# Kernel tuning notes

Measured on AMD Instinct MI355X. Metric: run time of the kernel, lower is better.

## Reference

```python
import jax, jax.numpy as jnp
import numpy as np

NUM_MOVIES = 100000
MOVIE_FEAT = 128
USER_FEAT = 128
BATCH = 16384
N_NBRS = 50
D0, D1, D2 = 256, 256, 128  # layer_dims


def setup_inputs() -> dict:
    key = jax.random.key(0)
    ks = jax.random.split(key, 16)
    inp = {
        "users": jax.random.normal(ks[0], (BATCH, USER_FEAT), jnp.float32),
        "pos_movies": jax.random.normal(ks[1], (BATCH, MOVIE_FEAT), jnp.float32),
        "neg_movies": jax.random.normal(ks[2], (BATCH, MOVIE_FEAT), jnp.float32),
        "user_ids": jax.random.randint(ks[3], (BATCH,), 0, BATCH),
        "pos_movie_ids": jax.random.randint(ks[4], (BATCH,), 0, NUM_MOVIES),
        "neg_movie_ids": jax.random.randint(ks[5], (BATCH,), 0, NUM_MOVIES),
        "nbr_ids": jax.random.randint(ks[6], (BATCH, N_NBRS), 0, NUM_MOVIES),
        # learned params / buffers
        "movie_table": jax.random.normal(ks[7], (NUM_MOVIES, MOVIE_FEAT), jnp.float32),
        "Wu": jax.random.normal(ks[8], (USER_FEAT, D0), jnp.float32) * (1.0 / np.sqrt(USER_FEAT)),
        "bu": jnp.zeros((D0,), jnp.float32),
        "Wm": jax.random.normal(ks[9], (MOVIE_FEAT, D0), jnp.float32) * (1.0 / np.sqrt(MOVIE_FEAT)),
        "bm": jnp.zeros((D0,), jnp.float32),
        "W1": jax.random.normal(ks[10], (D0, D1), jnp.float32) * (1.0 / np.sqrt(D0)),
        "b1": jnp.zeros((D1,), jnp.float32),
        "W2": jax.random.normal(ks[11], (D1, D2), jnp.float32) * (1.0 / np.sqrt(D1)),
        "b2": jnp.zeros((D2,), jnp.float32),
    }
    return inp


def reference(users, pos_movies, neg_movies, user_ids, pos_movie_ids, neg_movie_ids,
              nbr_ids, movie_table, Wu, bu, Wm, bm, W1, b1, W2, b2):
    # user_projection / movie_projection
    user_emb = users @ Wu + bu                      # [B, D0]
    movie_emb = movie_table @ Wm + bm               # [N, D0]
    pos_emb = movie_emb[pos_movie_ids]              # [B, D0]
    neg_emb = movie_emb[neg_movie_ids]              # [B, D0]
    # vectorized replacement of the per-user neighbor gather + mean loop
    nbr_mean = jnp.mean(movie_emb[nbr_ids], axis=1)  # [B, N_NBRS, D0] -> [B, D0]
    user_emb = user_emb + nbr_mean
    x = jnp.stack([user_emb, pos_emb, neg_emb], axis=0)  # [3, B, D0]
    x = jax.nn.relu(x @ W1 + b1)
    x = jax.nn.relu(x @ W2 + b2)
    return (x[0], x[1], x[2])
```

## Files before the change

kernel.cpp:

```cpp
#include <hip/hip_runtime.h>
#include <hip/hip_bf16.h>
#include <type_traits>

#define BATCH_N   16384
#define FEAT      128
#define NNBR      50
#define NUM_MOVIES_N 100000

typedef short  short8  __attribute__((ext_vector_type(8)));
typedef float  floatx4 __attribute__((ext_vector_type(4)));

__device__ __forceinline__ __hip_bfloat16 f2bf(float x) { return __float2bfloat16(x); }

__global__ __launch_bounds__(256) void conv_table(
    const float* __restrict__ t, __hip_bfloat16* __restrict__ tb) {
  size_t i = ((size_t)blockIdx.x * 256 + threadIdx.x) * 8;
  float4 v0 = *(const float4*)(t + i);
  float4 v1 = *(const float4*)(t + i + 4);
  __hip_bfloat16 o[8];
  o[0] = f2bf(v0.x); o[1] = f2bf(v0.y); o[2] = f2bf(v0.z); o[3] = f2bf(v0.w);
  o[4] = f2bf(v1.x); o[5] = f2bf(v1.y); o[6] = f2bf(v1.z); o[7] = f2bf(v1.w);
  *(short8*)(tb + i) = *(short8*)o;
}

__global__ __launch_bounds__(256) void prep_kernel(
    const float* __restrict__ Wu, const float* __restrict__ Wm,
    const float* __restrict__ W1, const float* __restrict__ W2,
    const float* __restrict__ bu, const float* __restrict__ bm,
    __hip_bfloat16* __restrict__ WcatT, __hip_bfloat16* __restrict__ WmT,
    __hip_bfloat16* __restrict__ W1T,  __hip_bfloat16* __restrict__ W2T,
    float* __restrict__ bc) {
  int idx = blockIdx.x * 256 + threadIdx.x;
  int n = idx & 255, k = idx >> 8;
  float v = (k < 128) ? Wu[k * 256 + n] : Wm[(k - 128) * 256 + n];
  WcatT[n * 256 + k] = f2bf(v);
  W1T[n * 256 + k]   = f2bf(W1[k * 256 + n]);
  if (k < 128) WmT[n * 128 + k] = f2bf(Wm[k * 256 + n]);
  if (idx < 32768) {
    int k2 = idx >> 7, n2 = idx & 127;
    W2T[n2 * 256 + k2] = f2bf(W2[k2 * 128 + n2]);
  }
  if (idx < 256) bc[idx] = bu[idx] + bm[idx];
}

__global__ __launch_bounds__(256) void gather_user(
    const float* __restrict__ users, const int* __restrict__ nbr_ids,
    const __hip_bfloat16* __restrict__ tb, __hip_bfloat16* __restrict__ A_user) {
  int row  = (blockIdx.x << 2) + (threadIdx.x >> 6);
  int lane = threadIdx.x & 63;
  const int* nb = nbr_ids + row * NNBR;
  float ax = 0.f, ay = 0.f;
  #pragma unroll 5
  for (int j = 0; j < NNBR; ++j) {
    int id = nb[j];
    __hip_bfloat162 v = ((const __hip_bfloat162*)(tb + (size_t)id * FEAT))[lane];
    ax += __bfloat162float(v.x); ay += __bfloat162float(v.y);
  }
  ax *= (1.f / NNBR); ay *= (1.f / NNBR);
  float2 uv = ((const float2*)(users + (size_t)row * FEAT))[lane];
  __hip_bfloat162* dst = (__hip_bfloat162*)(A_user + (size_t)row * (2 * FEAT));
  __hip_bfloat162 t0; t0.x = f2bf(uv.x); t0.y = f2bf(uv.y);
  __hip_bfloat162 t1; t1.x = f2bf(ax);   t1.y = f2bf(ay);
  dst[lane]      = t0;
  dst[64 + lane] = t1;
}

__global__ __launch_bounds__(256) void gather_pn(
    const int* __restrict__ pos_ids, const int* __restrict__ neg_ids,
    const __hip_bfloat16* __restrict__ tb, __hip_bfloat16* __restrict__ A_pn) {
  int row  = (blockIdx.x << 2) + (threadIdx.x >> 6);
  int lane = threadIdx.x & 63;
  int id = (row < BATCH_N) ? pos_ids[row] : neg_ids[row - BATCH_N];
  __hip_bfloat162 v = ((const __hip_bfloat162*)(tb + (size_t)id * FEAT))[lane];
  ((__hip_bfloat162*)(A_pn + (size_t)row * FEAT))[lane] = v;
}

template <int KDIM, int NDIM, bool RELU, typename OutT>
__global__ __launch_bounds__(256) void gemm_bf16(
    const __hip_bfloat16* __restrict__ A, const __hip_bfloat16* __restrict__ Wt,
    const float* __restrict__ bias, OutT* __restrict__ C) {
  __shared__ __hip_bfloat16 Al[128][40];
  __shared__ __hip_bfloat16 Bl[128][40];

  const int t    = threadIdx.x;
  const int lane = t & 63;
  const int wid  = t >> 6;
  const int wm   = wid & 1, wn = wid >> 1;
  const int quad = lane >> 4, lrow = lane & 15;
  const long m0  = (long)blockIdx.x * 128;
  const int  n0  = blockIdx.y * 128;

  const int c0 = t, c1 = t + 256;
  const int r0 = c0 >> 2, kc0 = (c0 & 3) * 8;
  const int r1 = c1 >> 2, kc1 = (c1 & 3) * 8;

  floatx4 acc[4][4] = {};

  for (int k0 = 0; k0 < KDIM; k0 += 32) {
    short8 a0 = *(const short8*)(A  + (m0 + r0) * KDIM + k0 + kc0);
    short8 a1 = *(const short8*)(A  + (m0 + r1) * KDIM + k0 + kc1);
    short8 b0 = *(const short8*)(Wt + (long)(n0 + r0) * KDIM + k0 + kc0);
    short8 b1 = *(const short8*)(Wt + (long)(n0 + r1) * KDIM + k0 + kc1);
    __syncthreads();
    *(short8*)&Al[r0][kc0] = a0;
    *(short8*)&Al[r1][kc1] = a1;
    *(short8*)&Bl[r0][kc0] = b0;
    *(short8*)&Bl[r1][kc1] = b1;
    __syncthreads();

    short8 af[4], bfr[4];
    #pragma unroll
    for (int i = 0; i < 4; ++i)
      af[i] = *(const short8*)&Al[wm * 64 + i * 16 + lrow][quad * 8];
    #pragma unroll
    for (int i = 0; i < 4; ++i)
      bfr[i] = *(const short8*)&Bl[wn * 64 + i * 16 + lrow][quad * 8];

    #pragma unroll
    for (int i = 0; i < 4; ++i)
      #pragma unroll
      for (int j = 0; j < 4; ++j)
        acc[i][j] = __builtin_amdgcn_mfma_f32_16x16x32_bf16(
            af[i], bfr[j], acc[i][j], 0, 0, 0);
  }

  #pragma unroll
  for (int i = 0; i < 4; ++i) {
    #pragma unroll
    for (int j = 0; j < 4; ++j) {
      int gcol = n0 + wn * 64 + j * 16 + lrow;
      float bv = bias[gcol];
      #pragma unroll
      for (int r = 0; r < 4; ++r) {
        long grow = m0 + wm * 64 + i * 16 + quad * 4 + r;
        float v = acc[i][j][r] + bv;
        if (RELU) v = fmaxf(v, 0.f);
        if constexpr (std::is_same<OutT, float>::value)
          C[grow * NDIM + gcol] = v;
        else
          C[grow * NDIM + gcol] = f2bf(v);
      }
    }
  }
}

extern "C" void kernel_launch(void* const* d_in, const int* in_sizes, int n_in,
                              void* d_out, int out_size, void* d_ws, size_t ws_size,
                              hipStream_t stream) {
  const float* users   = (const float*)d_in[0];
  const int*   pos_ids = (const int*)d_in[4];
  const int*   neg_ids = (const int*)d_in[5];
  const int*   nbr_ids = (const int*)d_in[6];
  const float* table   = (const float*)d_in[7];
  const float* Wu = (const float*)d_in[8];
  const float* bu = (const float*)d_in[9];
  const float* Wm = (const float*)d_in[10];
  const float* bm = (const float*)d_in[11];
  const float* W1 = (const float*)d_in[12];
  const float* b1 = (const float*)d_in[13];
  const float* W2 = (const float*)d_in[14];
  const float* b2 = (const float*)d_in[15];
  float* out = (float*)d_out;

  char* p = (char*)d_ws;
  auto carve = [&](size_t bytes) { char* r = p; p += (bytes + 255) & ~(size_t)255; return r; };
  __hip_bfloat16* tb     = (__hip_bfloat16*)carve((size_t)NUM_MOVIES_N * FEAT * 2);
  __hip_bfloat16* WcatT  = (__hip_bfloat16*)carve(256 * 256 * 2);
  __hip_bfloat16* WmT    = (__hip_bfloat16*)carve(256 * 128 * 2);
  __hip_bfloat16* W1T    = (__hip_bfloat16*)carve(256 * 256 * 2);
  __hip_bfloat16* W2T    = (__hip_bfloat16*)carve(128 * 256 * 2);
  float*          bc     = (float*)carve(256 * 4);
  __hip_bfloat16* A_user = (__hip_bfloat16*)carve((size_t)BATCH_N * 256 * 2);
  __hip_bfloat16* A_pn   = (__hip_bfloat16*)carve((size_t)2 * BATCH_N * 128 * 2);
  __hip_bfloat16* E      = (__hip_bfloat16*)carve((size_t)3 * BATCH_N * 256 * 2);
  __hip_bfloat16* H      = (__hip_bfloat16*)carve((size_t)3 * BATCH_N * 256 * 2);

  conv_table<<<NUM_MOVIES_N * FEAT / (256 * 8), 256, 0, stream>>>(table, tb);
  prep_kernel<<<256, 256, 0, stream>>>(Wu, Wm, W1, W2, bu, bm,
                                       WcatT, WmT, W1T, W2T, bc);
  gather_user<<<BATCH_N / 4, 256, 0, stream>>>(users, nbr_ids, tb, A_user);
  gather_pn<<<2 * BATCH_N / 4, 256, 0, stream>>>(pos_ids, neg_ids, tb, A_pn);

  gemm_bf16<256, 256, false, __hip_bfloat16>
      <<<dim3(BATCH_N / 128, 2), 256, 0, stream>>>(A_user, WcatT, bc, E);
  gemm_bf16<128, 256, false, __hip_bfloat16>
      <<<dim3(2 * BATCH_N / 128, 2), 256, 0, stream>>>(A_pn, WmT, bm,
                                                       E + (size_t)BATCH_N * 256);
  gemm_bf16<256, 256, true, __hip_bfloat16>
      <<<dim3(3 * BATCH_N / 128, 2), 256, 0, stream>>>(E, W1T, b1, H);
  gemm_bf16<256, 128, true, float>
      <<<dim3(3 * BATCH_N / 128, 1), 256, 0, stream>>>(H, W2T, b2, out);
}
```

Measured before the change: 218.3 us.

## Fuse pos/neg gather and three GEMM layers into one LDS-resident MLP kernel

Replaces the pos/neg gather kernel and the four separate GEMM launches with a single fused kernel. Each block holds a 64-row tile in LDS across projection, layer 1 and layer 2, and gathers pos/neg rows from the bf16 table inside the kernel. Intermediate E and H activations therefore never go to global memory, and several launches are removed. Weights are now read directly from global/L2 per MFMA fragment instead of being staged in LDS. An XOR swizzle is used for LDS indexing to avoid bank conflicts. The trade-off is heavier weight traffic from cache and 64 KB of LDS per block, which limits occupancy.

```diff
diff --git a/kernel.cpp b/kernel.cpp
--- a/kernel.cpp
+++ b/kernel.cpp
@@ -1,6 +1,5 @@
 #include <hip/hip_runtime.h>
 #include <hip/hip_bf16.h>
-#include <type_traits>
 
 #define BATCH_N   16384
 #define FEAT      128
@@ -11,6 +10,10 @@
 typedef float  floatx4 __attribute__((ext_vector_type(4)));
 
 __device__ __forceinline__ __hip_bfloat16 f2bf(float x) { return __float2bfloat16(x); }
+
+__device__ __forceinline__ int sw_idx(int r, int c) {
+  return (r << 8) + ((((c >> 3) ^ (r & 7)) << 3) | (c & 7));
+}
 
 __global__ __launch_bounds__(256) void conv_table(
     const float* __restrict__ t, __hip_bfloat16* __restrict__ tb) {
@@ -65,81 +68,142 @@
   dst[64 + lane] = t1;
 }
 
-__global__ __launch_bounds__(256) void gather_pn(
+__global__ __launch_bounds__(256, 2) void fused_mlp(
+    const __hip_bfloat16* __restrict__ A_user,
+    const __hip_bfloat16* __restrict__ tb,
     const int* __restrict__ pos_ids, const int* __restrict__ neg_ids,
-    const __hip_bfloat16* __restrict__ tb, __hip_bfloat16* __restrict__ A_pn) {
-  int row  = (blockIdx.x << 2) + (threadIdx.x >> 6);
-  int lane = threadIdx.x & 63;
-  int id = (row < BATCH_N) ? pos_ids[row] : neg_ids[row - BATCH_N];
-  __hip_bfloat162 v = ((const __hip_bfloat162*)(tb + (size_t)id * FEAT))[lane];
-  ((__hip_bfloat162*)(A_pn + (size_t)row * FEAT))[lane] = v;
-}
-
-template <int KDIM, int NDIM, bool RELU, typename OutT>
-__global__ __launch_bounds__(256) void gemm_bf16(
-    const __hip_bfloat16* __restrict__ A, const __hip_bfloat16* __restrict__ Wt,
-    const float* __restrict__ bias, OutT* __restrict__ C) {
-  __shared__ __hip_bfloat16 Al[128][40];
-  __shared__ __hip_bfloat16 Bl[128][40];
+    const __hip_bfloat16* __restrict__ WcatT,
+    const __hip_bfloat16* __restrict__ WmT,
+    const __hip_bfloat16* __restrict__ W1T,
+    const __hip_bfloat16* __restrict__ W2T,
+    const float* __restrict__ bc, const float* __restrict__ bmv,
+    const float* __restrict__ b1, const float* __restrict__ b2,
+    float* __restrict__ out) {
+  __shared__ __hip_bfloat16 A_lds[64 * 256];
+  __shared__ __hip_bfloat16 E_lds[64 * 256];
 
   const int t    = threadIdx.x;
-  const int lane = t & 63;
-  const int wid  = t >> 6;
+  const int lane = t & 63, wid = t >> 6;
   const int wm   = wid & 1, wn = wid >> 1;
   const int quad = lane >> 4, lrow = lane & 15;
-  const long m0  = (long)blockIdx.x * 128;
-  const int  n0  = blockIdx.y * 128;
-
-  const int c0 = t, c1 = t + 256;
-  const int r0 = c0 >> 2, kc0 = (c0 & 3) * 8;
-  const int r1 = c1 >> 2, kc1 = (c1 & 3) * 8;
-
-  floatx4 acc[4][4] = {};
-
-  for (int k0 = 0; k0 < KDIM; k0 += 32) {
-    short8 a0 = *(const short8*)(A  + (m0 + r0) * KDIM + k0 + kc0);
-    short8 a1 = *(const short8*)(A  + (m0 + r1) * KDIM + k0 + kc1);
-    short8 b0 = *(const short8*)(Wt + (long)(n0 + r0) * KDIM + k0 + kc0);
-    short8 b1 = *(const short8*)(Wt + (long)(n0 + r1) * KDIM + k0 + kc1);
-    __syncthreads();
-    *(short8*)&Al[r0][kc0] = a0;
-    *(short8*)&Al[r1][kc1] = a1;
-    *(short8*)&Bl[r0][kc0] = b0;
-    *(short8*)&Bl[r1][kc1] = b1;
-    __syncthreads();
-
-    short8 af[4], bfr[4];
-    #pragma unroll
-    for (int i = 0; i < 4; ++i)
-      af[i] = *(const short8*)&Al[wm * 64 + i * 16 + lrow][quad * 8];
-    #pragma unroll
-    for (int i = 0; i < 4; ++i)
-      bfr[i] = *(const short8*)&Bl[wn * 64 + i * 16 + lrow][quad * 8];
-
-    #pragma unroll
-    for (int i = 0; i < 4; ++i)
-      #pragma unroll
-      for (int j = 0; j < 4; ++j)
-        acc[i][j] = __builtin_amdgcn_mfma_f32_16x16x32_bf16(
-            af[i], bfr[j], acc[i][j], 0, 0, 0);
-  }
-
-  #pragma unroll
-  for (int i = 0; i < 4; ++i) {
+  const int s    = blockIdx.y;
+  const int m0   = blockIdx.x * 64;
+
+  if (s == 0) {
+    #pragma unroll
+    for (int c = 0; c < 8; ++c) {
+      int ch = t + c * 256;
+      int r = ch >> 5, kc = (ch & 31) << 3;
+      *(short8*)&A_lds[sw_idx(r, kc)] =
+          *(const short8*)(A_user + ((size_t)(m0 + r) << 8) + kc);
+    }
+  } else {
+    const int* ids = (s == 1) ? pos_ids : neg_ids;
+    #pragma unroll
+    for (int c = 0; c < 4; ++c) {
+      int ch = t + c * 256;
+      int r = ch >> 4, kc = (ch & 15) << 3;
+      int id = ids[m0 + r];
+      *(short8*)&A_lds[sw_idx(r, kc)] =
+          *(const short8*)(tb + ((size_t)id << 7) + kc);
+    }
+  }
+  __syncthreads();
+
+  const __hip_bfloat16* W0 = (s == 0) ? WcatT : WmT;
+  const float* bias0 = (s == 0) ? bc : bmv;
+  const int K0 = (s == 0) ? 256 : 128;
+
+  {
+    floatx4 acc[2][8] = {};
+    for (int k0 = 0; k0 < K0; k0 += 32) {
+      short8 af[2];
+      #pragma unroll
+      for (int i = 0; i < 2; ++i)
+        af[i] = *(const short8*)&A_lds[sw_idx(wm * 32 + i * 16 + lrow, k0 + quad * 8)];
+      #pragma unroll
+      for (int j = 0; j < 8; ++j) {
+        int n = wn * 128 + j * 16 + lrow;
+        short8 bf = *(const short8*)(W0 + (size_t)n * K0 + k0 + quad * 8);
+        #pragma unroll
+        for (int i = 0; i < 2; ++i)
+          acc[i][j] = __builtin_amdgcn_mfma_f32_16x16x32_bf16(af[i], bf, acc[i][j], 0, 0, 0);
+      }
+    }
+    #pragma unroll
+    for (int j = 0; j < 8; ++j) {
+      int col = wn * 128 + j * 16 + lrow;
+      float bv = bias0[col];
+      #pragma unroll
+      for (int i = 0; i < 2; ++i)
+        #pragma unroll
+        for (int r = 0; r < 4; ++r) {
+          int row = wm * 32 + i * 16 + quad * 4 + r;
+          E_lds[sw_idx(row, col)] = f2bf(acc[i][j][r] + bv);
+        }
+    }
+  }
+  __syncthreads();
+
+  {
+    floatx4 acc[2][8] = {};
+    for (int k0 = 0; k0 < 256; k0 += 32) {
+      short8 af[2];
+      #pragma unroll
+      for (int i = 0; i < 2; ++i)
+        af[i] = *(const short8*)&E_lds[sw_idx(wm * 32 + i * 16 + lrow, k0 + quad * 8)];
+      #pragma unroll
+      for (int j = 0; j < 8; ++j) {
+        int n = wn * 128 + j * 16 + lrow;
+        short8 bf = *(const short8*)(W1T + ((size_t)n << 8) + k0 + quad * 8);
+        #pragma unroll
+        for (int i = 0; i < 2; ++i)
+          acc[i][j] = __builtin_amdgcn_mfma_f32_16x16x32_bf16(af[i], bf, acc[i][j], 0, 0, 0);
+      }
+    }
+    #pragma unroll
+    for (int j = 0; j < 8; ++j) {
+      int col = wn * 128 + j * 16 + lrow;
+      float bv = b1[col];
+      #pragma unroll
+      for (int i = 0; i < 2; ++i)
+        #pragma unroll
+        for (int r = 0; r < 4; ++r) {
+          int row = wm * 32 + i * 16 + quad * 4 + r;
+          A_lds[sw_idx(row, col)] = f2bf(fmaxf(acc[i][j][r] + bv, 0.f));
+        }
+    }
+  }
+  __syncthreads();
+
+  {
+    floatx4 acc[2][4] = {};
+    for (int k0 = 0; k0 < 256; k0 += 32) {
+      short8 af[2];
+      #pragma unroll
+      for (int i = 0; i < 2; ++i)
+        af[i] = *(const short8*)&A_lds[sw_idx(wm * 32 + i * 16 + lrow, k0 + quad * 8)];
+      #pragma unroll
+      for (int j = 0; j < 4; ++j) {
+        int n = wn * 64 + j * 16 + lrow;
+        short8 bf = *(const short8*)(W2T + ((size_t)n << 8) + k0 + quad * 8);
+        #pragma unroll
+        for (int i = 0; i < 2; ++i)
+          acc[i][j] = __builtin_amdgcn_mfma_f32_16x16x32_bf16(af[i], bf, acc[i][j], 0, 0, 0);
+      }
+    }
     #pragma unroll
     for (int j = 0; j < 4; ++j) {
-      int gcol = n0 + wn * 64 + j * 16 + lrow;
-      float bv = bias[gcol];
-      #pragma unroll
-      for (int r = 0; r < 4; ++r) {
-        long grow = m0 + wm * 64 + i * 16 + quad * 4 + r;
-        float v = acc[i][j][r] + bv;
-        if (RELU) v = fmaxf(v, 0.f);
-        if constexpr (std::is_same<OutT, float>::value)
-          C[grow * NDIM + gcol] = v;
-        else
-          C[grow * NDIM + gcol] = f2bf(v);
-      }
+      int col = wn * 64 + j * 16 + lrow;
+      float bv = b2[col];
+      #pragma unroll
+      for (int i = 0; i < 2; ++i)
+        #pragma unroll
+        for (int r = 0; r < 4; ++r) {
+          int row = wm * 32 + i * 16 + quad * 4 + r;
+          float v = fmaxf(acc[i][j][r] + bv, 0.f);
+          out[((size_t)s * BATCH_N + m0 + row) * 128 + col] = v;
+        }
     }
   }
 }
@@ -171,23 +235,12 @@
   __hip_bfloat16* W2T    = (__hip_bfloat16*)carve(128 * 256 * 2);
   float*          bc     = (float*)carve(256 * 4);
   __hip_bfloat16* A_user = (__hip_bfloat16*)carve((size_t)BATCH_N * 256 * 2);
-  __hip_bfloat16* A_pn   = (__hip_bfloat16*)carve((size_t)2 * BATCH_N * 128 * 2);
-  __hip_bfloat16* E      = (__hip_bfloat16*)carve((size_t)3 * BATCH_N * 256 * 2);
-  __hip_bfloat16* H      = (__hip_bfloat16*)carve((size_t)3 * BATCH_N * 256 * 2);
 
   conv_table<<<NUM_MOVIES_N * FEAT / (256 * 8), 256, 0, stream>>>(table, tb);
   prep_kernel<<<256, 256, 0, stream>>>(Wu, Wm, W1, W2, bu, bm,
                                        WcatT, WmT, W1T, W2T, bc);
   gather_user<<<BATCH_N / 4, 256, 0, stream>>>(users, nbr_ids, tb, A_user);
-  gather_pn<<<2 * BATCH_N / 4, 256, 0, stream>>>(pos_ids, neg_ids, tb, A_pn);
-
-  gemm_bf16<256, 256, false, __hip_bfloat16>
-      <<<dim3(BATCH_N / 128, 2), 256, 0, stream>>>(A_user, WcatT, bc, E);
-  gemm_bf16<128, 256, false, __hip_bfloat16>
-      <<<dim3(2 * BATCH_N / 128, 2), 256, 0, stream>>>(A_pn, WmT, bm,
-                                                       E + (size_t)BATCH_N * 256);
-  gemm_bf16<256, 256, true, __hip_bfloat16>
-      <<<dim3(3 * BATCH_N / 128, 2), 256, 0, stream>>>(E, W1T, b1, H);
-  gemm_bf16<256, 128, true, float>
-      <<<dim3(3 * BATCH_N / 128, 1), 256, 0, stream>>>(H, W2T, b2, out);
-}
+  fused_mlp<<<dim3(BATCH_N / 64, 3), 256, 0, stream>>>(
+      A_user, tb, pos_ids, neg_ids, WcatT, WmT, W1T, W2T,
+      bc, bm, b1, b2, out);
+}
```

New measurement: 219.1 us. No clear change (+0.4%).
